# Kernel tuning notes

Measured on AMD Instinct MI355X. Metric: run time of the kernel, lower is better.

The kernel has to match this reference:

```python
import jax, jax.numpy as jnp
import numpy as np

B, T_ENC, T_OUT = 64, 1024, 1000
N_MELS, ENC_D, DEC_H, ATTN_D = 80, 256, 256, 256


def setup_inputs() -> dict:
    key = jax.random.key(0)
    ks = jax.random.split(key, 24)

    def p(k, shape, scale=0.05):
        return jax.random.normal(k, shape, dtype=jnp.float32) * scale

    lengths = jax.random.randint(ks[0], (B,), T_ENC // 2, T_ENC + 1)
    enc_mask = (jnp.arange(T_ENC)[None, :] < lengths[:, None]).astype(jnp.float32)
    return {
        "enc_outputs": jax.random.normal(ks[1], (B, T_ENC, ENC_D), dtype=jnp.float32),
        "target_mel": jax.random.normal(ks[2], (B, T_OUT, N_MELS), dtype=jnp.float32),
        # attention params
        "W_enc": p(ks[3], (ATTN_D, ENC_D)), "b_enc": jnp.zeros((ATTN_D,), jnp.float32),
        "W_dec": p(ks[4], (ATTN_D, DEC_H)), "b_dec": jnp.zeros((ATTN_D,), jnp.float32),
        "v_w": p(ks[5], (1, ATTN_D)), "v_b": jnp.zeros((1,), jnp.float32),
        # prenet
        "pre_W1": p(ks[6], (DEC_H, N_MELS)), "pre_b1": jnp.zeros((DEC_H,), jnp.float32),
        "pre_W2": p(ks[7], (DEC_H, DEC_H)), "pre_b2": jnp.zeros((DEC_H,), jnp.float32),
        # LSTMCell (PyTorch gate order i, f, g, o)
        "W_ih": p(ks[8], (4 * DEC_H, DEC_H + ENC_D)), "W_hh": p(ks[9], (4 * DEC_H, DEC_H)),
        "b_ih": jnp.zeros((4 * DEC_H,), jnp.float32), "b_hh": jnp.zeros((4 * DEC_H,), jnp.float32),
        # output heads
        "mel_W": p(ks[10], (N_MELS, DEC_H + ENC_D)), "mel_b": jnp.zeros((N_MELS,), jnp.float32),
        "stop_W": p(ks[11], (1, DEC_H + ENC_D)), "stop_b": jnp.zeros((1,), jnp.float32),
        "enc_mask": enc_mask,
    }


def reference(enc_outputs, target_mel, W_enc, b_enc, W_dec, b_dec, v_w, v_b,
              pre_W1, pre_b1, pre_W2, pre_b2, W_ih, W_hh, b_ih, b_hh,
              mel_W, mel_b, stop_W, stop_b, enc_mask):
    Bsz = enc_outputs.shape[0]
    H = W_hh.shape[1]
    NEG = jnp.float32(-1e9)
    # precompute encoder projection once, as the original does
    attn_enc = jnp.einsum('bte,ae->bta', enc_outputs, W_enc) + b_enc  # (B, T_enc, A)
    # teacher forcing: input at step t is target_mel[t-1], zeros at t=0
    prev_inputs = jnp.concatenate(
        [jnp.zeros_like(target_mel[:, :1]), target_mel[:, :-1]], axis=1)
    xs = jnp.swapaxes(prev_inputs, 0, 1)  # (T_out, B, n_mels)

    def step(carry, prev):
        h, c = carry
        attn_dec = h @ W_dec.T + b_dec                                  # (B, A)
        energy = jnp.tanh(attn_enc + attn_dec[:, None, :]) @ v_w[0] + v_b[0]  # (B, T_enc)
        energy = jnp.where(enc_mask == 0, NEG, energy)
        attn = jax.nn.softmax(energy, axis=-1)
        context = jnp.einsum('bt,btd->bd', attn, enc_outputs)           # (B, enc_d)
        pre = jax.nn.relu(prev @ pre_W1.T + pre_b1)                     # dropout = identity (eval)
        pre = jax.nn.relu(pre @ pre_W2.T + pre_b2)
        x = jnp.concatenate([pre, context], axis=1)
        gates = x @ W_ih.T + b_ih + h @ W_hh.T + b_hh                   # (B, 4H)
        i, f, g, o = jnp.split(gates, 4, axis=1)
        c_new = jax.nn.sigmoid(f) * c + jax.nn.sigmoid(i) * jnp.tanh(g)
        h_new = jax.nn.sigmoid(o) * jnp.tanh(c_new)
        comb = jnp.concatenate([h_new, context], axis=1)
        mel = comb @ mel_W.T + mel_b
        stop = (comb @ stop_W.T + stop_b)[:, 0]
        return (h_new, c_new), (mel, stop)

    h0 = jnp.zeros((Bsz, H), dtype=enc_outputs.dtype)
    _, (mels, stops) = jax.lax.scan(step, (h0, h0), xs)
    return jnp.swapaxes(mels, 0, 1), jnp.swapaxes(stops, 0, 1)
```

## Files before the change

kernel.cpp:

```cpp
#include <hip/hip_runtime.h>
#include <hip/hip_bf16.h>

#define NMEL 80

__device__ __forceinline__ float bf2f(unsigned short u) {
  unsigned v = ((unsigned)u) << 16; float f; __builtin_memcpy(&f, &v, 4); return f;
}
__device__ __forceinline__ unsigned short f2bf_u(float f) {
  __hip_bfloat16 h = __float2bfloat16(f); unsigned short u; __builtin_memcpy(&u, &h, 2); return u;
}
__device__ __forceinline__ float agload(const float* p) {
  return __hip_atomic_load(p, __ATOMIC_RELAXED, __HIP_MEMORY_SCOPE_AGENT);
}
__device__ __forceinline__ void agstore(float* p, float v) {
  __hip_atomic_store(p, v, __ATOMIC_RELAXED, __HIP_MEMORY_SCOPE_AGENT);
}
__device__ __forceinline__ void unpk(unsigned u, float& lo, float& hi) {
  unsigned l = u << 16, h = u & 0xffff0000u;
  __builtin_memcpy(&lo, &l, 4); __builtin_memcpy(&hi, &h, 4);
}
__device__ __forceinline__ void pin_u(unsigned& x) { asm volatile("" : "+v"(x)); }

constexpr size_t OFF_ATTNR = 0;
constexpr size_t SZ_ATTNR = (size_t)64 * 256 * 1024 * 2;
constexpr size_t OFF_ENCBF = OFF_ATTNR + SZ_ATTNR;
constexpr size_t SZ_ENCBF = (size_t)64 * 1024 * 256 * 2;
constexpr size_t OFF_PRE2 = OFF_ENCBF + SZ_ENCBF;
constexpr size_t SZ_PRE2 = (size_t)64000 * 256 * 2;
constexpr size_t OFF_WG4 = OFF_PRE2 + SZ_PRE2;
constexpr size_t SZ_W4 = (size_t)262144 * 4;
constexpr size_t OFF_WP4 = OFF_WG4 + SZ_W4;
constexpr size_t OFF_WHH4 = OFF_WP4 + SZ_W4;
constexpr size_t OFF_WDEC4 = OFF_WHH4 + SZ_W4;
constexpr size_t SZ_WDEC4 = (size_t)65536 * 4;
constexpr size_t OFF_MELT = OFF_WDEC4 + SZ_WDEC4;
constexpr size_t SZ_MELT = (size_t)4 * 128 * 80 * 4;
constexpr size_t OFF_STOPT = OFF_MELT + SZ_MELT;
constexpr size_t SZ_STOPT = (size_t)4 * 128 * 4;
constexpr size_t OFF_BIASG = OFF_STOPT + SZ_STOPT;
constexpr size_t SZ_BIASG = (size_t)4 * 256 * 4;
constexpr size_t OFF_EXCH = (OFF_BIASG + SZ_BIASG + 255) & ~(size_t)255;
constexpr size_t EXF_DEC = 0;
constexpr size_t EXN_DEC = (size_t)2 * 64 * 4 * 256;
constexpr size_t EXF_GH = EXF_DEC + EXN_DEC;
constexpr size_t EXN_GH = (size_t)2 * 64 * 4 * 1024;
constexpr size_t EXF_CTX = EXF_GH + EXN_GH;
constexpr size_t EXN_CTX = (size_t)64 * 4 * 256;
constexpr size_t EXF_S = EXF_CTX + EXN_CTX;
constexpr size_t EXN_S = 64 * 16;
constexpr size_t EXF_CTR = EXF_S + EXN_S;
constexpr size_t EXN_CTR = 64 * 16;
constexpr size_t EXCH_FLOATS = EXF_CTR + EXN_CTR;
constexpr size_t SZ_EXCH = EXCH_FLOATS * 4;
constexpr size_t WS_NEED = OFF_EXCH + SZ_EXCH;

__global__ __launch_bounds__(256) void conv_bf16(const float* __restrict__ in,
                                                 unsigned short* __restrict__ out, int n) {
  int i = (blockIdx.x * 256 + threadIdx.x) * 2;
  if (i < n) {
    float2 v = *(const float2*)(in + i);
    unsigned pair = (unsigned)f2bf_u(v.x) | ((unsigned)f2bf_u(v.y) << 16);
    *(unsigned*)(out + i) = pair;
  }
}

__global__ __launch_bounds__(256) void prep_weights(
    const float* __restrict__ W_ih, const float* __restrict__ W_hh,
    const float* __restrict__ W_dec, const float* __restrict__ mel_W,
    const float* __restrict__ stop_W, const float* __restrict__ b_ih,
    const float* __restrict__ b_hh,
    float* __restrict__ Wg4, float* __restrict__ Wp4,
    float* __restrict__ Whh4, float* __restrict__ Wdec4,
    float* __restrict__ MelT, float* __restrict__ StopT, float* __restrict__ biasG) {
  int idx = blockIdx.x * 256 + threadIdx.x;
  if (idx < 262144) {
    int q = idx & 3, r = (idx >> 2) & 255, kq = (idx >> 10) & 63, s = idx >> 16;
    int grow = ((r >> 6) << 8) + s * 64 + (r & 63);
    Wg4[idx] = W_ih[(size_t)grow * 512 + 256 + kq * 4 + q];
    Wp4[idx] = W_ih[(size_t)grow * 512 + kq * 4 + q];
  } else if (idx < 524288) {
    int i = idx - 262144;
    int q = i & 3, rr = (i >> 2) & 1023, hq = (i >> 12) & 15, s = i >> 16;
    Whh4[i] = W_hh[(size_t)rr * 256 + s * 64 + hq * 4 + q];
  } else if (idx < 589824) {
    int i = idx - 524288;
    int q = i & 3, a = (i >> 2) & 255, hq = (i >> 10) & 15, s = (i >> 14) & 3;
    Wdec4[i] = W_dec[(size_t)a * 256 + s * 64 + hq * 4 + q];
  } else if (idx < 589824 + 40960) {
    int k = idx - 589824;
    int m = k % 80, r = k / 80;
    int cc = r & 127, s = r >> 7;
    int col = (cc < 64) ? (s * 64 + cc) : (256 + s * 64 + (cc - 64));
    MelT[k] = mel_W[(size_t)m * 512 + col];
  } else if (idx < 589824 + 40960 + 512) {
    int k = idx - (589824 + 40960);
    int cc = k & 127, s = k >> 7;
    int col = (cc < 64) ? (s * 64 + cc) : (256 + s * 64 + (cc - 64));
    StopT[k] = stop_W[col];
  } else if (idx < 589824 + 40960 + 512 + 1024) {
    int k = idx - (589824 + 40960 + 512);
    int j = k & 255, s = k >> 8;
    int row = ((j >> 6) << 8) + s * 64 + (j & 63);
    biasG[k] = b_ih[row] + b_hh[row];
  }
}

__global__ __launch_bounds__(256) void attn_gemm(const float* __restrict__ enc,
                                                 const float* __restrict__ W_enc,
                                                 const float* __restrict__ b_enc,
                                                 unsigned* __restrict__ attnR) {
  __shared__ unsigned short Alds[64 * 260];
  const int tid = threadIdx.x;
  const int row0 = blockIdx.x * 64;
  const int wv = tid >> 6, lane = tid & 63, nb = wv * 64;
  for (int idx = tid; idx < 64 * 256; idx += 256) {
    int r = idx >> 8, k = idx & 255;
    Alds[r * 260 + k] = f2bf_u(enc[(size_t)(row0 + r) * 256 + k]);
  }
  __syncthreads();
  float acc[64];
#pragma unroll
  for (int n = 0; n < 64; ++n) acc[n] = b_enc[nb + n];
  for (int k8 = 0; k8 < 256; k8 += 8) {
    ushort4 ua = *(const ushort4*)&Alds[lane * 260 + k8];
    ushort4 ub = *(const ushort4*)&Alds[lane * 260 + k8 + 4];
    float a0 = bf2f(ua.x), a1 = bf2f(ua.y), a2 = bf2f(ua.z), a3 = bf2f(ua.w);
    float a4 = bf2f(ub.x), a5 = bf2f(ub.y), a6 = bf2f(ub.z), a7 = bf2f(ub.w);
#pragma unroll
    for (int n = 0; n < 64; ++n) {
      const float4* wp = (const float4*)(W_enc + (size_t)(nb + n) * 256 + k8);
      float4 w0 = wp[0], w1 = wp[1];
      acc[n] = fmaf(a0, w0.x, acc[n]); acc[n] = fmaf(a1, w0.y, acc[n]);
      acc[n] = fmaf(a2, w0.z, acc[n]); acc[n] = fmaf(a3, w0.w, acc[n]);
      acc[n] = fmaf(a4, w1.x, acc[n]); acc[n] = fmaf(a5, w1.y, acc[n]);
      acc[n] = fmaf(a6, w1.z, acc[n]); acc[n] = fmaf(a7, w1.w, acc[n]);
    }
  }
  const float CE = 2.8853900817779268f;
  const int b = row0 >> 10;
  const int te_g = (row0 & 1023) + lane;
  const int sl = te_g >> 8, te_loc = te_g & 255;
#pragma unroll
  for (int n = 0; n < 64; n += 2) {
    int a = nb + n;
    unsigned pair = (unsigned)f2bf_u(acc[n] * CE) | ((unsigned)f2bf_u(acc[n + 1] * CE) << 16);
    size_t u4 = ((((size_t)(b * 4 + sl) * 4 + (a >> 6)) * 8 + ((a >> 3) & 7)) * 256 + te_loc);
    attnR[u4 * 4 + ((a & 7) >> 1)] = pair;
  }
}

__global__ __launch_bounds__(256) void prenet_fused(const float* __restrict__ tmel,
                                                    const float* __restrict__ W1,
                                                    const float* __restrict__ b1,
                                                    const float* __restrict__ W2,
                                                    const float* __restrict__ b2,
                                                    unsigned short* __restrict__ pre2) {
  __shared__ unsigned short Alds[64 * 260];
  const int tid = threadIdx.x;
  const int row0 = blockIdx.x * 64;
  const int wv = tid >> 6, lane = tid & 63, nb = wv * 64;
  for (int idx = tid; idx < 64 * 80; idx += 256) {
    int r = idx / 80, k = idx - r * 80;
    int R = row0 + r;
    float v = (R % 1000 != 0) ? tmel[(size_t)(R - 1) * NMEL + k] : 0.f;
    Alds[r * 260 + k] = f2bf_u(v);
  }
  __syncthreads();
  float acc[64];
#pragma unroll
  for (int n = 0; n < 64; ++n) acc[n] = b1[nb + n];
  for (int k8 = 0; k8 < 80; k8 += 8) {
    ushort4 ua = *(const ushort4*)&Alds[lane * 260 + k8];
    ushort4 ub = *(const ushort4*)&Alds[lane * 260 + k8 + 4];
    float a0 = bf2f(ua.x), a1 = bf2f(ua.y), a2 = bf2f(ua.z), a3 = bf2f(ua.w);
    float a4 = bf2f(ub.x), a5 = bf2f(ub.y), a6 = bf2f(ub.z), a7 = bf2f(ub.w);
#pragma unroll
    for (int n = 0; n < 64; ++n) {
      const float4* wp = (const float4*)(W1 + (size_t)(nb + n) * 80 + k8);
      float4 w0 = wp[0], w1 = wp[1];
      acc[n] = fmaf(a0, w0.x, acc[n]); acc[n] = fmaf(a1, w0.y, acc[n]);
      acc[n] = fmaf(a2, w0.z, acc[n]); acc[n] = fmaf(a3, w0.w, acc[n]);
      acc[n] = fmaf(a4, w1.x, acc[n]); acc[n] = fmaf(a5, w1.y, acc[n]);
      acc[n] = fmaf(a6, w1.z, acc[n]); acc[n] = fmaf(a7, w1.w, acc[n]);
    }
  }
  __syncthreads();
#pragma unroll
  for (int n = 0; n < 64; ++n) Alds[lane * 260 + nb + n] = f2bf_u(fmaxf(acc[n], 0.f));
  __syncthreads();
#pragma unroll
  for (int n = 0; n < 64; ++n) acc[n] = b2[nb + n];
  for (int k8 = 0; k8 < 256; k8 += 8) {
    ushort4 ua = *(const ushort4*)&Alds[lane * 260 + k8];
    ushort4 ub = *(const ushort4*)&Alds[lane * 260 + k8 + 4];
    float a0 = bf2f(ua.x), a1 = bf2f(ua.y), a2 = bf2f(ua.z), a3 = bf2f(ua.w);
    float a4 = bf2f(ub.x), a5 = bf2f(ub.y), a6 = bf2f(ub.z), a7 = bf2f(ub.w);
#pragma unroll
    for (int n = 0; n < 64; ++n) {
      const float4* wp = (const float4*)(W2 + (size_t)(nb + n) * 256 + k8);
      float4 w0 = wp[0], w1 = wp[1];
      acc[n] = fmaf(a0, w0.x, acc[n]); acc[n] = fmaf(a1, w0.y, acc[n]);
      acc[n] = fmaf(a2, w0.z, acc[n]); acc[n] = fmaf(a3, w0.w, acc[n]);
      acc[n] = fmaf(a4, w1.x, acc[n]); acc[n] = fmaf(a5, w1.y, acc[n]);
      acc[n] = fmaf(a6, w1.z, acc[n]); acc[n] = fmaf(a7, w1.w, acc[n]);
    }
  }
  __syncthreads();
#pragma unroll
  for (int n = 0; n < 64; ++n) Alds[lane * 260 + nb + n] = f2bf_u(fmaxf(acc[n], 0.f));
  __syncthreads();
  for (int idx = tid; idx < 64 * 128; idx += 256) {
    int r = idx >> 7, k2 = (idx & 127) * 2;
    unsigned pair = (unsigned)Alds[r * 260 + k2] | ((unsigned)Alds[r * 260 + k2 + 1] << 16);
    *(unsigned*)(pre2 + (size_t)(row0 + r) * 256 + k2) = pair;
  }
}

__global__ __launch_bounds__(1024, 4) void decoder_loop(
    const unsigned* __restrict__ attnR, const unsigned short* __restrict__ encbf,
    const unsigned short* __restrict__ pre2,
    const float* __restrict__ Wg4, const float* __restrict__ Wp4,
    const float* __restrict__ Whh4, const float* __restrict__ Wdec4,
    const float* __restrict__ MelT, const float* __restrict__ StopT,
    const float* __restrict__ biasG,
    float* exch, unsigned* ctr,
    const float* __restrict__ b_dec, const float* __restrict__ v_w,
    const float* __restrict__ v_b, const float* __restrict__ enc_mask,
    const float* __restrict__ mel_b, const float* __restrict__ stop_b,
    float* out) {
  __shared__ __align__(16) float scratch[4096];
  __shared__ __align__(16) float melT_lds[10240];
  __shared__ float stopT_lds[128];
  __shared__ __align__(16) float dec_lds[256];
  __shared__ __align__(16) float v2_lds[256];
  __shared__ __align__(16) float p_lds[256];
  __shared__ __align__(16) float ctx_lds[256];
  __shared__ __align__(16) float pre_lds[256];
  __shared__ float gates_lds[256];
  __shared__ float c_lds[64], h_lds[64];
  __shared__ float red_lds[16];
  __shared__ float sv_lds;

  const int tid = threadIdx.x;
  const int b = blockIdx.x & 63, s = blockIdx.x >> 6;
  const int t8 = tid & 255;
  const int chunk = tid >> 8;
  const int lane = tid & 63, wid = tid >> 6;
  const int w = tid >> 6;
  const float CE = 2.8853900817779268f;
  const float L2E = 1.4426950408889634f;

  if (tid < 256) {
    v2_lds[tid] = -2.f * v_w[tid];
    if (tid < 64) c_lds[tid] = 0.f;
    float sp = v_w[tid];
    for (int m = 32; m; m >>= 1) sp += __shfl_xor(sp, m);
    if (lane == 0) red_lds[wid] = sp;
  }
  for (int i = tid; i < 10240; i += 1024) melT_lds[i] = MelT[(size_t)s * 10240 + i];
  if (tid >= 512 && tid < 640) stopT_lds[tid - 512] = StopT[s * 128 + (tid - 512)];
  __syncthreads();
  if (tid == 0) sv_lds = red_lds[0] + red_lds[1] + red_lds[2] + red_lds[3];
  __syncthreads();
  const float Sv = sv_lds;
  const float vb = v_b[0];
  const float maskv = (tid < 256) ? enc_mask[b * 1024 + s * 256 + tid] : 0.f;
  const float bdec_r = (tid < 256) ? b_dec[tid] : 0.f;
  const float biasg_r = (tid < 256) ? biasG[s * 256 + tid] : 0.f;

  uint4 attn_r4[8];
  {
    const uint4* apR = (const uint4*)attnR + (((size_t)(b * 4 + s) * 4 + chunk) * 8) * 256 + t8;
#pragma unroll
    for (int j = 0; j < 8; ++j) attn_r4[j] = apR[(size_t)j << 8];
  }
  uint2 enc_r2[16];
  {
    const uint2* epR = (const uint2*)encbf + ((size_t)(b * 1024 + s * 256 + w * 16)) * 64 + lane;
#pragma unroll
    for (int t = 0; t < 16; ++t) enc_r2[t] = epR[(size_t)t << 6];
  }
#pragma unroll
  for (int j = 0; j < 8; ++j) {
    pin_u(attn_r4[j].x); pin_u(attn_r4[j].y); pin_u(attn_r4[j].z); pin_u(attn_r4[j].w);
  }
#pragma unroll
  for (int t = 0; t < 16; ++t) { pin_u(enc_r2[t].x); pin_u(enc_r2[t].y); }

  const int grow = ((t8 >> 6) << 8) + s * 64 + (t8 & 63);
  const float4* wg4 = (const float4*)Wg4 + ((size_t)(s * 64 + chunk * 16)) * 256 + t8;
  const float4* wp4 = (const float4*)Wp4 + ((size_t)(s * 64 + chunk * 16)) * 256 + t8;
  const float4* wh4 = (const float4*)Whh4 + ((size_t)s) * 16384 + tid;
  const float4* wd4 = (const float4*)Wdec4 + ((size_t)(s * 16 + chunk * 4)) * 256 + t8;
  const unsigned short* pre2_b = pre2 + (size_t)b * 256000;

  float* decP = exch + EXF_DEC;
  float* ghP = exch + EXF_GH;
  float* ctxP = exch + EXF_CTX;
  float* sP = exch + EXF_S;
  unsigned* ctrb = ctr + b * 16;
  unsigned epoch = 0;

  for (int it = 0; it < 1000; ++it) {
    const int par = it & 1;
    const int pn = par ^ 1;
    float prefv = (tid < 256) ? bf2f(pre2_b[it * 256 + tid]) : 0.f;
    scratch[tid] = agload(decP + ((size_t)(par * 64 + b)) * 1024 + tid);
    __syncthreads();
    if (tid < 256)
      dec_lds[tid] = (bdec_r + scratch[tid] + scratch[256 + tid] + scratch[512 + tid] +
                      scratch[768 + tid]) * CE;
    __syncthreads();
    {
      float acc = 0.f;
#pragma unroll
      for (int j = 0; j < 8; ++j) {
        uint4 u = attn_r4[j];
        int ab = chunk * 64 + j * 8;
        float4 d0 = *(const float4*)&dec_lds[ab];
        float4 d1 = *(const float4*)&dec_lds[ab + 4];
        float4 v0 = *(const float4*)&v2_lds[ab];
        float4 v1 = *(const float4*)&v2_lds[ab + 4];
        float t0, t1, t2, t3, t4, t5, t6, t7;
        unpk(u.x, t0, t1); unpk(u.y, t2, t3); unpk(u.z, t4, t5); unpk(u.w, t6, t7);
        acc = fmaf(v0.x, __builtin_amdgcn_rcpf(1.f + __builtin_amdgcn_exp2f(t0 + d0.x)), acc);
        acc = fmaf(v0.y, __builtin_amdgcn_rcpf(1.f + __builtin_amdgcn_exp2f(t1 + d0.y)), acc);
        acc = fmaf(v0.z, __builtin_amdgcn_rcpf(1.f + __builtin_amdgcn_exp2f(t2 + d0.z)), acc);
        acc = fmaf(v0.w, __builtin_amdgcn_rcpf(1.f + __builtin_amdgcn_exp2f(t3 + d0.w)), acc);
        acc = fmaf(v1.x, __builtin_amdgcn_rcpf(1.f + __builtin_amdgcn_exp2f(t4 + d1.x)), acc);
        acc = fmaf(v1.y, __builtin_amdgcn_rcpf(1.f + __builtin_amdgcn_exp2f(t5 + d1.y)), acc);
        acc = fmaf(v1.z, __builtin_amdgcn_rcpf(1.f + __builtin_amdgcn_exp2f(t6 + d1.z)), acc);
        acc = fmaf(v1.w, __builtin_amdgcn_rcpf(1.f + __builtin_amdgcn_exp2f(t7 + d1.w)), acc);
      }
      scratch[tid] = acc;
    }
    __syncthreads();
    if (tid < 256) {
      float e = Sv + vb + scratch[t8] + scratch[256 + t8] + scratch[512 + t8] + scratch[768 + t8];
      float p = (maskv != 0.f) ? __builtin_amdgcn_exp2f(e * L2E) : 0.f;
      p_lds[t8] = p;
      float sp = p;
      for (int m = 32; m; m >>= 1) sp += __shfl_xor(sp, m);
      if (lane == 0) red_lds[wid] = sp;
    }
    __syncthreads();
    {
      float c0 = 0, c1 = 0, c2 = 0, c3 = 0;
#pragma unroll
      for (int t = 0; t < 16; ++t) {
        float pv = p_lds[w * 16 + t];
        float e0, e1, e2, e3;
        unpk(enc_r2[t].x, e0, e1);
        unpk(enc_r2[t].y, e2, e3);
        c0 = fmaf(pv, e0, c0); c1 = fmaf(pv, e1, c1);
        c2 = fmaf(pv, e2, c2); c3 = fmaf(pv, e3, c3);
      }
      float* cb = &scratch[w * 256 + lane * 4];
      cb[0] = c0; cb[1] = c1; cb[2] = c2; cb[3] = c3;
      if (tid < 256) pre_lds[tid] = prefv;
    }
    __syncthreads();
    if (tid < 256) {
      float cp = 0.f;
#pragma unroll
      for (int ww = 0; ww < 16; ++ww) cp += scratch[ww * 256 + t8];
      agstore(ctxP + ((size_t)b * 4 + s) * 256 + t8, cp);
    }
    if (tid == 0)
      agstore(sP + b * 16 + s, red_lds[0] + red_lds[1] + red_lds[2] + red_lds[3]);
    __threadfence();
    __syncthreads();
    if (tid == 0) {
      ++epoch;
      __hip_atomic_fetch_add(ctrb, 1u, __ATOMIC_RELEASE, __HIP_MEMORY_SCOPE_AGENT);
      while (__hip_atomic_load(ctrb, __ATOMIC_ACQUIRE, __HIP_MEMORY_SCOPE_AGENT) < 4u * epoch)
        __builtin_amdgcn_s_sleep(1);
    }
    __syncthreads();
    scratch[tid] = agload(ctxP + ((size_t)b * 4 + chunk) * 256 + t8);
    if (tid < 4) red_lds[8 + tid] = agload(sP + b * 16 + tid);
    __syncthreads();
    if (tid < 256) {
      float rS = 1.f / (red_lds[8] + red_lds[9] + red_lds[10] + red_lds[11]);
      ctx_lds[t8] = (scratch[t8] + scratch[256 + t8] + scratch[512 + t8] + scratch[768 + t8]) * rS;
    }
    __syncthreads();
    {
      float g = agload(ghP + ((size_t)(par * 64 + b)) * 4096 + chunk * 1024 + grow);
#pragma unroll 8
      for (int i = 0; i < 16; ++i) {
        float4 wv = wg4[(size_t)i << 8];
        float4 qv = wp4[(size_t)i << 8];
        int kb = chunk * 64 + i * 4;
        float4 x = *(const float4*)&ctx_lds[kb];
        float4 y = *(const float4*)&pre_lds[kb];
        g = fmaf(wv.x, x.x, g); g = fmaf(wv.y, x.y, g);
        g = fmaf(wv.z, x.z, g); g = fmaf(wv.w, x.w, g);
        g = fmaf(qv.x, y.x, g); g = fmaf(qv.y, y.y, g);
        g = fmaf(qv.z, y.z, g); g = fmaf(qv.w, y.w, g);
      }
      scratch[tid] = g;
    }
    __syncthreads();
    if (tid < 256)
      gates_lds[t8] = biasg_r + scratch[t8] + scratch[256 + t8] + scratch[512 + t8] +
                      scratch[768 + t8];
    __syncthreads();
    if (tid < 64) {
      float ii = gates_lds[tid], ff = gates_lds[64 + tid];
      float gg = gates_lds[128 + tid], oo = gates_lds[192 + tid];
      float c = c_lds[tid];
      float si = __builtin_amdgcn_rcpf(1.f + __builtin_amdgcn_exp2f(-ii * L2E));
      float sf = __builtin_amdgcn_rcpf(1.f + __builtin_amdgcn_exp2f(-ff * L2E));
      float so = __builtin_amdgcn_rcpf(1.f + __builtin_amdgcn_exp2f(-oo * L2E));
      float tg2 = 1.f - 2.f * __builtin_amdgcn_rcpf(1.f + __builtin_amdgcn_exp2f(gg * CE));
      float cn = sf * c + si * tg2;
      float tc = 1.f - 2.f * __builtin_amdgcn_rcpf(1.f + __builtin_amdgcn_exp2f(cn * CE));
      c_lds[tid] = cn;
      h_lds[tid] = so * tc;
    }
    __syncthreads();
    if (tid < 80) {
      float a = (s == 0) ? mel_b[tid] : 0.f;
#pragma unroll 8
      for (int cc = 0; cc < 128; ++cc) {
        float xv = (cc < 64) ? h_lds[cc] : ctx_lds[s * 64 + (cc - 64)];
        a = fmaf(melT_lds[cc * 80 + tid], xv, a);
      }
      atomicAdd(&out[(size_t)b * 80000 + it * 80 + tid], a);
    }
    if (tid >= 512 && tid < 640) {
      int cc = tid - 512;
      float xv = (cc < 64) ? h_lds[cc] : ctx_lds[s * 64 + (cc - 64)];
      float sv2 = stopT_lds[cc] * xv;
      for (int m = 32; m; m >>= 1) sv2 += __shfl_xor(sv2, m);
      if (lane == 0) red_lds[12 + ((tid - 512) >> 6)] = sv2;
    }
    {
      float gd = 0.f;
#pragma unroll
      for (int i = 0; i < 4; ++i) {
        float4 wv = wd4[(size_t)i << 8];
        int hb = chunk * 16 + i * 4;
        gd = fmaf(wv.x, h_lds[hb + 0], gd); gd = fmaf(wv.y, h_lds[hb + 1], gd);
        gd = fmaf(wv.z, h_lds[hb + 2], gd); gd = fmaf(wv.w, h_lds[hb + 3], gd);
      }
      float gh = 0.f;
#pragma unroll 8
      for (int hq = 0; hq < 16; ++hq) {
        float4 wv = wh4[(size_t)hq << 10];
        gh = fmaf(wv.x, h_lds[hq * 4 + 0], gh); gh = fmaf(wv.y, h_lds[hq * 4 + 1], gh);
        gh = fmaf(wv.z, h_lds[hq * 4 + 2], gh); gh = fmaf(wv.w, h_lds[hq * 4 + 3], gh);
      }
      agstore(ghP + ((size_t)(pn * 64 + b) * 4 + s) * 1024 + tid, gh);
      scratch[tid] = gd;
    }
    __syncthreads();
    if (tid < 256)
      agstore(decP + ((size_t)(pn * 64 + b) * 4 + s) * 256 + t8,
              scratch[t8] + scratch[256 + t8] + scratch[512 + t8] + scratch[768 + t8]);
    if (tid == 0) {
      float st = (s == 0) ? stop_b[0] : 0.f;
      atomicAdd(&out[(size_t)5120000 + b * 1000 + it], st + red_lds[12] + red_lds[13]);
    }
    __threadfence();
    __syncthreads();
    if (tid == 0) {
      ++epoch;
      __hip_atomic_fetch_add(ctrb, 1u, __ATOMIC_RELEASE, __HIP_MEMORY_SCOPE_AGENT);
      while (__hip_atomic_load(ctrb, __ATOMIC_ACQUIRE, __HIP_MEMORY_SCOPE_AGENT) < 4u * epoch)
        __builtin_amdgcn_s_sleep(1);
    }
    __syncthreads();
  }
}

extern "C" void kernel_launch(void* const* d_in, const int* in_sizes, int n_in,
                              void* d_out, int out_size, void* d_ws, size_t ws_size,
                              hipStream_t stream) {
  const float* enc = (const float*)d_in[0];
  const float* tmel = (const float*)d_in[1];
  const float* W_enc = (const float*)d_in[2];
  const float* b_enc = (const float*)d_in[3];
  const float* W_dec = (const float*)d_in[4];
  const float* b_dec = (const float*)d_in[5];
  const float* v_w = (const float*)d_in[6];
  const float* v_b = (const float*)d_in[7];
  const float* pW1 = (const float*)d_in[8];
  const float* pb1 = (const float*)d_in[9];
  const float* pW2 = (const float*)d_in[10];
  const float* pb2 = (const float*)d_in[11];
  const float* W_ih = (const float*)d_in[12];
  const float* W_hh = (const float*)d_in[13];
  const float* b_ih = (const float*)d_in[14];
  const float* b_hh = (const float*)d_in[15];
  const float* mel_W = (const float*)d_in[16];
  const float* mel_b = (const float*)d_in[17];
  const float* stop_W = (const float*)d_in[18];
  const float* stop_b = (const float*)d_in[19];
  const float* emask = (const float*)d_in[20];

  if (ws_size < WS_NEED) return;

  char* ws = (char*)d_ws;
  unsigned* attnR = (unsigned*)(ws + OFF_ATTNR);
  unsigned short* encbf = (unsigned short*)(ws + OFF_ENCBF);
  unsigned short* pre2 = (unsigned short*)(ws + OFF_PRE2);
  float* Wg4 = (float*)(ws + OFF_WG4);
  float* Wp4 = (float*)(ws + OFF_WP4);
  float* Whh4 = (float*)(ws + OFF_WHH4);
  float* Wdec4 = (float*)(ws + OFF_WDEC4);
  float* MelT = (float*)(ws + OFF_MELT);
  float* StopT = (float*)(ws + OFF_STOPT);
  float* biasG = (float*)(ws + OFF_BIASG);
  float* exch = (float*)(ws + OFF_EXCH);
  unsigned* ctr = (unsigned*)(exch + EXF_CTR);

  hipMemsetAsync(exch, 0, SZ_EXCH, stream);
  hipMemsetAsync(d_out, 0, (size_t)out_size * 4, stream);

  conv_bf16<<<32768, 256, 0, stream>>>(enc, encbf, 64 * 1024 * 256);
  prep_weights<<<2470, 256, 0, stream>>>(W_ih, W_hh, W_dec, mel_W, stop_W, b_ih, b_hh,
                                         Wg4, Wp4, Whh4, Wdec4, MelT, StopT, biasG);
  attn_gemm<<<1024, 256, 0, stream>>>(enc, W_enc, b_enc, attnR);
  prenet_fused<<<1000, 256, 0, stream>>>(tmel, pW1, pb1, pW2, pb2, pre2);
  decoder_loop<<<256, 1024, 0, stream>>>(attnR, encbf, pre2, Wg4, Wp4, Whh4, Wdec4,
                                         MelT, StopT, biasG, exch, ctr, b_dec, v_w, v_b,
                                         emask, mel_b, stop_b, (float*)d_out);
}
```

Measured before the change: 168.6 ms.

## Run each batch decoder in one workgroup, dropping cross-block counter barriers

Measured after the change: 178.2 ms. +5.7%, slower.

```diff
diff --git a/kernel.cpp b/kernel.cpp
--- a/kernel.cpp
+++ b/kernel.cpp
@@ -3,105 +3,75 @@
 
 #define NMEL 80
 
+typedef unsigned u32x4 __attribute__((ext_vector_type(4)));
+
 __device__ __forceinline__ float bf2f(unsigned short u) {
   unsigned v = ((unsigned)u) << 16; float f; __builtin_memcpy(&f, &v, 4); return f;
 }
 __device__ __forceinline__ unsigned short f2bf_u(float f) {
   __hip_bfloat16 h = __float2bfloat16(f); unsigned short u; __builtin_memcpy(&u, &h, 2); return u;
-}
-__device__ __forceinline__ float agload(const float* p) {
-  return __hip_atomic_load(p, __ATOMIC_RELAXED, __HIP_MEMORY_SCOPE_AGENT);
-}
-__device__ __forceinline__ void agstore(float* p, float v) {
-  __hip_atomic_store(p, v, __ATOMIC_RELAXED, __HIP_MEMORY_SCOPE_AGENT);
 }
 __device__ __forceinline__ void unpk(unsigned u, float& lo, float& hi) {
   unsigned l = u << 16, h = u & 0xffff0000u;
   __builtin_memcpy(&lo, &l, 4); __builtin_memcpy(&hi, &h, 4);
 }
-__device__ __forceinline__ void pin_u(unsigned& x) { asm volatile("" : "+v"(x)); }
 
 constexpr size_t OFF_ATTNR = 0;
-constexpr size_t SZ_ATTNR = (size_t)64 * 256 * 1024 * 2;
-constexpr size_t OFF_ENCBF = OFF_ATTNR + SZ_ATTNR;
-constexpr size_t SZ_ENCBF = (size_t)64 * 1024 * 256 * 2;
-constexpr size_t OFF_PRE2 = OFF_ENCBF + SZ_ENCBF;
+constexpr size_t SZ_ATTNR = (size_t)64 * 1024 * 256 * 2;
+constexpr size_t OFF_ENCP = OFF_ATTNR + SZ_ATTNR;
+constexpr size_t SZ_ENCP = (size_t)64 * 1024 * 256 * 2;
+constexpr size_t OFF_PRE2 = OFF_ENCP + SZ_ENCP;
 constexpr size_t SZ_PRE2 = (size_t)64000 * 256 * 2;
-constexpr size_t OFF_WG4 = OFF_PRE2 + SZ_PRE2;
-constexpr size_t SZ_W4 = (size_t)262144 * 4;
-constexpr size_t OFF_WP4 = OFF_WG4 + SZ_W4;
-constexpr size_t OFF_WHH4 = OFF_WP4 + SZ_W4;
-constexpr size_t OFF_WDEC4 = OFF_WHH4 + SZ_W4;
-constexpr size_t SZ_WDEC4 = (size_t)65536 * 4;
-constexpr size_t OFF_MELT = OFF_WDEC4 + SZ_WDEC4;
-constexpr size_t SZ_MELT = (size_t)4 * 128 * 80 * 4;
-constexpr size_t OFF_STOPT = OFF_MELT + SZ_MELT;
-constexpr size_t SZ_STOPT = (size_t)4 * 128 * 4;
-constexpr size_t OFF_BIASG = OFF_STOPT + SZ_STOPT;
-constexpr size_t SZ_BIASG = (size_t)4 * 256 * 4;
-constexpr size_t OFF_EXCH = (OFF_BIASG + SZ_BIASG + 255) & ~(size_t)255;
-constexpr size_t EXF_DEC = 0;
-constexpr size_t EXN_DEC = (size_t)2 * 64 * 4 * 256;
-constexpr size_t EXF_GH = EXF_DEC + EXN_DEC;
-constexpr size_t EXN_GH = (size_t)2 * 64 * 4 * 1024;
-constexpr size_t EXF_CTX = EXF_GH + EXN_GH;
-constexpr size_t EXN_CTX = (size_t)64 * 4 * 256;
-constexpr size_t EXF_S = EXF_CTX + EXN_CTX;
-constexpr size_t EXN_S = 64 * 16;
-constexpr size_t EXF_CTR = EXF_S + EXN_S;
-constexpr size_t EXN_CTR = 64 * 16;
-constexpr size_t EXCH_FLOATS = EXF_CTR + EXN_CTR;
-constexpr size_t SZ_EXCH = EXCH_FLOATS * 4;
-constexpr size_t WS_NEED = OFF_EXCH + SZ_EXCH;
-
-__global__ __launch_bounds__(256) void conv_bf16(const float* __restrict__ in,
-                                                 unsigned short* __restrict__ out, int n) {
-  int i = (blockIdx.x * 256 + threadIdx.x) * 2;
-  if (i < n) {
-    float2 v = *(const float2*)(in + i);
-    unsigned pair = (unsigned)f2bf_u(v.x) | ((unsigned)f2bf_u(v.y) << 16);
-    *(unsigned*)(out + i) = pair;
-  }
-}
-
-__global__ __launch_bounds__(256) void prep_weights(
-    const float* __restrict__ W_ih, const float* __restrict__ W_hh,
-    const float* __restrict__ W_dec, const float* __restrict__ mel_W,
-    const float* __restrict__ stop_W, const float* __restrict__ b_ih,
+constexpr size_t OFF_WDT = OFF_PRE2 + SZ_PRE2;
+constexpr size_t SZ_WDT = (size_t)65536 * 4;
+constexpr size_t OFF_WHT = OFF_WDT + SZ_WDT;
+constexpr size_t SZ_W1M = (size_t)262144 * 4;
+constexpr size_t OFF_WCT = OFF_WHT + SZ_W1M;
+constexpr size_t OFF_WPT = OFF_WCT + SZ_W1M;
+constexpr size_t OFF_BIASG = OFF_WPT + SZ_W1M;
+constexpr size_t SZ_BIASG = 1024 * 4;
+constexpr size_t WS_NEED = OFF_BIASG + SZ_BIASG;
+
+__global__ __launch_bounds__(256) void conv_encP(const float* __restrict__ enc,
+                                                 u32x4* __restrict__ encP) {
+  int idx = blockIdx.x * 256 + threadIdx.x;
+  int b = idx >> 15, r = idx & 32767;
+  int d8 = r >> 10, te = r & 1023;
+  const float4* src = (const float4*)(enc + ((size_t)(b * 1024 + te)) * 256 + d8 * 8);
+  float4 x0 = src[0], x1 = src[1];
+  u32x4 o;
+  o.x = (unsigned)f2bf_u(x0.x) | ((unsigned)f2bf_u(x0.y) << 16);
+  o.y = (unsigned)f2bf_u(x0.z) | ((unsigned)f2bf_u(x0.w) << 16);
+  o.z = (unsigned)f2bf_u(x1.x) | ((unsigned)f2bf_u(x1.y) << 16);
+  o.w = (unsigned)f2bf_u(x1.z) | ((unsigned)f2bf_u(x1.w) << 16);
+  encP[((size_t)(b * 32 + d8)) * 1024 + te] = o;
+}
+
+__global__ __launch_bounds__(256) void prep_w2(
+    const float* __restrict__ W_dec, const float* __restrict__ W_hh,
+    const float* __restrict__ W_ih, const float* __restrict__ b_ih,
     const float* __restrict__ b_hh,
-    float* __restrict__ Wg4, float* __restrict__ Wp4,
-    float* __restrict__ Whh4, float* __restrict__ Wdec4,
-    float* __restrict__ MelT, float* __restrict__ StopT, float* __restrict__ biasG) {
+    float* __restrict__ WdT, float* __restrict__ WhT,
+    float* __restrict__ WcT, float* __restrict__ WpT, float* __restrict__ biasG) {
   int idx = blockIdx.x * 256 + threadIdx.x;
-  if (idx < 262144) {
-    int q = idx & 3, r = (idx >> 2) & 255, kq = (idx >> 10) & 63, s = idx >> 16;
-    int grow = ((r >> 6) << 8) + s * 64 + (r & 63);
-    Wg4[idx] = W_ih[(size_t)grow * 512 + 256 + kq * 4 + q];
-    Wp4[idx] = W_ih[(size_t)grow * 512 + kq * 4 + q];
-  } else if (idx < 524288) {
-    int i = idx - 262144;
-    int q = i & 3, rr = (i >> 2) & 1023, hq = (i >> 12) & 15, s = i >> 16;
-    Whh4[i] = W_hh[(size_t)rr * 256 + s * 64 + hq * 4 + q];
+  if (idx < 65536) {
+    int q = idx & 3, a = (idx >> 2) & 255, kq = idx >> 10;
+    WdT[idx] = W_dec[(size_t)a * 256 + kq * 4 + q];
+  } else if (idx < 327680) {
+    int i = idx - 65536;
+    int q = i & 3, g = (i >> 2) & 1023, kq = i >> 12;
+    WhT[i] = W_hh[(size_t)g * 256 + kq * 4 + q];
   } else if (idx < 589824) {
-    int i = idx - 524288;
-    int q = i & 3, a = (i >> 2) & 255, hq = (i >> 10) & 15, s = (i >> 14) & 3;
-    Wdec4[i] = W_dec[(size_t)a * 256 + s * 64 + hq * 4 + q];
-  } else if (idx < 589824 + 40960) {
-    int k = idx - 589824;
-    int m = k % 80, r = k / 80;
-    int cc = r & 127, s = r >> 7;
-    int col = (cc < 64) ? (s * 64 + cc) : (256 + s * 64 + (cc - 64));
-    MelT[k] = mel_W[(size_t)m * 512 + col];
-  } else if (idx < 589824 + 40960 + 512) {
-    int k = idx - (589824 + 40960);
-    int cc = k & 127, s = k >> 7;
-    int col = (cc < 64) ? (s * 64 + cc) : (256 + s * 64 + (cc - 64));
-    StopT[k] = stop_W[col];
-  } else if (idx < 589824 + 40960 + 512 + 1024) {
-    int k = idx - (589824 + 40960 + 512);
-    int j = k & 255, s = k >> 8;
-    int row = ((j >> 6) << 8) + s * 64 + (j & 63);
-    biasG[k] = b_ih[row] + b_hh[row];
+    int i = idx - 327680;
+    int q = i & 3, g = (i >> 2) & 1023, kq = i >> 12;
+    WcT[i] = W_ih[(size_t)g * 512 + 256 + kq * 4 + q];
+  } else if (idx < 851968) {
+    int i = idx - 589824;
+    int q = i & 3, g = (i >> 2) & 1023, kq = i >> 12;
+    WpT[i] = W_ih[(size_t)g * 512 + kq * 4 + q];
+  } else if (idx < 852992) {
+    int g = idx - 851968;
+    biasG[g] = b_ih[g] + b_hh[g];
   }
 }
 
@@ -216,107 +186,122 @@
   }
 }
 
-__global__ __launch_bounds__(1024, 4) void decoder_loop(
-    const unsigned* __restrict__ attnR, const unsigned short* __restrict__ encbf,
+__global__ __launch_bounds__(1024, 4) void decoder_one(
+    const u32x4* __restrict__ attnR, const u32x4* __restrict__ encP,
     const unsigned short* __restrict__ pre2,
-    const float* __restrict__ Wg4, const float* __restrict__ Wp4,
-    const float* __restrict__ Whh4, const float* __restrict__ Wdec4,
-    const float* __restrict__ MelT, const float* __restrict__ StopT,
+    const float4* __restrict__ WdT, const float4* __restrict__ WhT,
+    const float4* __restrict__ WcT, const float4* __restrict__ WpT,
     const float* __restrict__ biasG,
-    float* exch, unsigned* ctr,
     const float* __restrict__ b_dec, const float* __restrict__ v_w,
     const float* __restrict__ v_b, const float* __restrict__ enc_mask,
-    const float* __restrict__ mel_b, const float* __restrict__ stop_b,
-    float* out) {
-  __shared__ __align__(16) float scratch[4096];
-  __shared__ __align__(16) float melT_lds[10240];
-  __shared__ float stopT_lds[128];
+    const float* __restrict__ mel_W, const float* __restrict__ mel_b,
+    const float* __restrict__ stop_W, const float* __restrict__ stop_b,
+    float* __restrict__ out) {
+  __shared__ __align__(16) float scratchB[8448];
+  __shared__ __align__(16) float p_lds[1024];
+  __shared__ __align__(16) float gates_lds[1024];
+  __shared__ __align__(16) float h_lds[256];
+  __shared__ __align__(16) float ctx_lds[256];
+  __shared__ __align__(16) float pre_lds[256];
   __shared__ __align__(16) float dec_lds[256];
   __shared__ __align__(16) float v2_lds[256];
-  __shared__ __align__(16) float p_lds[256];
-  __shared__ __align__(16) float ctx_lds[256];
-  __shared__ __align__(16) float pre_lds[256];
-  __shared__ float gates_lds[256];
-  __shared__ float c_lds[64], h_lds[64];
   __shared__ float red_lds[16];
-  __shared__ float sv_lds;
 
   const int tid = threadIdx.x;
-  const int b = blockIdx.x & 63, s = blockIdx.x >> 6;
-  const int t8 = tid & 255;
-  const int chunk = tid >> 8;
+  const int b = blockIdx.x;
+  const int t8 = tid & 255, chunk = tid >> 8;
   const int lane = tid & 63, wid = tid >> 6;
-  const int w = tid >> 6;
+  const int d8 = tid >> 5, tec = tid & 31;
   const float CE = 2.8853900817779268f;
   const float L2E = 1.4426950408889634f;
 
   if (tid < 256) {
-    v2_lds[tid] = -2.f * v_w[tid];
-    if (tid < 64) c_lds[tid] = 0.f;
-    float sp = v_w[tid];
-    for (int m = 32; m; m >>= 1) sp += __shfl_xor(sp, m);
-    if (lane == 0) red_lds[wid] = sp;
-  }
-  for (int i = tid; i < 10240; i += 1024) melT_lds[i] = MelT[(size_t)s * 10240 + i];
-  if (tid >= 512 && tid < 640) stopT_lds[tid - 512] = StopT[s * 128 + (tid - 512)];
-  __syncthreads();
-  if (tid == 0) sv_lds = red_lds[0] + red_lds[1] + red_lds[2] + red_lds[3];
-  __syncthreads();
-  const float Sv = sv_lds;
-  const float vb = v_b[0];
-  const float maskv = (tid < 256) ? enc_mask[b * 1024 + s * 256 + tid] : 0.f;
+    h_lds[tid] = 0.f;
+    float v = v_w[tid];
+    v2_lds[tid] = -2.f * v;
+    for (int m = 32; m; m >>= 1) v += __shfl_xor(v, m);
+    if (lane == 0) red_lds[wid] = v;
+  }
+  float c_reg = 0.f;
+  const float maskv = enc_mask[b * 1024 + tid];
   const float bdec_r = (tid < 256) ? b_dec[tid] : 0.f;
-  const float biasg_r = (tid < 256) ? biasG[s * 256 + tid] : 0.f;
-
-  uint4 attn_r4[8];
-  {
-    const uint4* apR = (const uint4*)attnR + (((size_t)(b * 4 + s) * 4 + chunk) * 8) * 256 + t8;
-#pragma unroll
-    for (int j = 0; j < 8; ++j) attn_r4[j] = apR[(size_t)j << 8];
-  }
-  uint2 enc_r2[16];
-  {
-    const uint2* epR = (const uint2*)encbf + ((size_t)(b * 1024 + s * 256 + w * 16)) * 64 + lane;
-#pragma unroll
-    for (int t = 0; t < 16; ++t) enc_r2[t] = epR[(size_t)t << 6];
-  }
-#pragma unroll
-  for (int j = 0; j < 8; ++j) {
-    pin_u(attn_r4[j].x); pin_u(attn_r4[j].y); pin_u(attn_r4[j].z); pin_u(attn_r4[j].w);
-  }
-#pragma unroll
-  for (int t = 0; t < 16; ++t) { pin_u(enc_r2[t].x); pin_u(enc_r2[t].y); }
-
-  const int grow = ((t8 >> 6) << 8) + s * 64 + (t8 & 63);
-  const float4* wg4 = (const float4*)Wg4 + ((size_t)(s * 64 + chunk * 16)) * 256 + t8;
-  const float4* wp4 = (const float4*)Wp4 + ((size_t)(s * 64 + chunk * 16)) * 256 + t8;
-  const float4* wh4 = (const float4*)Whh4 + ((size_t)s) * 16384 + tid;
-  const float4* wd4 = (const float4*)Wdec4 + ((size_t)(s * 16 + chunk * 4)) * 256 + t8;
+  const float biasg_r = biasG[tid];
+  const float melb_r = (tid < 640 && (tid & 7) == 0) ? mel_b[tid >> 3] : 0.f;
+  float stopw[8];
+  if (wid == 11) {
+#pragma unroll
+    for (int i = 0; i < 8; ++i) stopw[i] = stop_W[lane * 8 + i];
+  }
+  __syncthreads();
+  const float Sv_vb = red_lds[0] + red_lds[1] + red_lds[2] + red_lds[3] + v_b[0];
+  const float stopb0 = stop_b[0];
+
+  const u32x4* aB = attnR + (size_t)b * 32768 + chunk * 2048 + t8;
+  const u32x4* eB = encP + ((size_t)(b * 32 + d8)) * 1024 + tec;
+  const float4* wdB = WdT + chunk * 16 * 256 + t8;
+  const float4* whB = WhT + tid;
+  const float4* wcB = WcT + tid;
+  const float4* wpB = WpT + tid;
   const unsigned short* pre2_b = pre2 + (size_t)b * 256000;
-
-  float* decP = exch + EXF_DEC;
-  float* ghP = exch + EXF_GH;
-  float* ctxP = exch + EXF_CTX;
-  float* sP = exch + EXF_S;
-  unsigned* ctrb = ctr + b * 16;
-  unsigned epoch = 0;
+  float* outm = out + (size_t)b * 80000;
+  float* outs = out + (size_t)5120000 + b * 1000;
+
+  auto heads = [&](int ith) {
+    if (tid < 640) {
+      const int m = tid >> 3, q = tid & 7;
+      float acc = melb_r;
+      const float4* wm = (const float4*)(mel_W + (size_t)m * 512 + q * 64);
+      const float4* xp = (q < 4) ? (const float4*)&h_lds[q * 64]
+                                 : (const float4*)&ctx_lds[(q - 4) * 64];
+#pragma unroll
+      for (int i = 0; i < 16; ++i) {
+        float4 w = wm[i]; float4 x = xp[i];
+        acc = fmaf(w.x, x.x, acc); acc = fmaf(w.y, x.y, acc);
+        acc = fmaf(w.z, x.z, acc); acc = fmaf(w.w, x.w, acc);
+      }
+      acc += __shfl_xor(acc, 1); acc += __shfl_xor(acc, 2); acc += __shfl_xor(acc, 4);
+      if (q == 0) outm[ith * 80 + m] = acc;
+    } else if (wid == 11) {
+      float acc = 0.f;
+#pragma unroll
+      for (int i = 0; i < 8; ++i) {
+        int cc = lane * 8 + i;
+        float x = (cc < 256) ? h_lds[cc] : ctx_lds[cc - 256];
+        acc = fmaf(stopw[i], x, acc);
+      }
+      for (int m = 32; m; m >>= 1) acc += __shfl_xor(acc, m);
+      if (lane == 0) outs[ith] = acc + stopb0;
+    }
+  };
+
+  float gph = 0.f;
 
   for (int it = 0; it < 1000; ++it) {
-    const int par = it & 1;
-    const int pn = par ^ 1;
-    float prefv = (tid < 256) ? bf2f(pre2_b[it * 256 + tid]) : 0.f;
-    scratch[tid] = agload(decP + ((size_t)(par * 64 + b)) * 1024 + tid);
-    __syncthreads();
-    if (tid < 256)
-      dec_lds[tid] = (bdec_r + scratch[tid] + scratch[256 + tid] + scratch[512 + tid] +
-                      scratch[768 + tid]) * CE;
-    __syncthreads();
     {
       float acc = 0.f;
 #pragma unroll
+      for (int i = 0; i < 16; ++i) {
+        float4 w = wdB[(size_t)i << 8];
+        float4 h4 = *(const float4*)&h_lds[chunk * 64 + i * 4];
+        acc = fmaf(w.x, h4.x, acc); acc = fmaf(w.y, h4.y, acc);
+        acc = fmaf(w.z, h4.z, acc); acc = fmaf(w.w, h4.w, acc);
+      }
+      scratchB[(chunk << 8) + t8] = acc;
+      if (tid < 256) pre_lds[tid] = bf2f(pre2_b[it * 256 + tid]);
+      if (it > 0) heads(it - 1);
+    }
+    __syncthreads();
+    if (tid < 256)
+      dec_lds[tid] = (bdec_r + scratchB[tid] + scratchB[256 + tid] +
+                      scratchB[512 + tid] + scratchB[768 + tid]) * CE;
+    __syncthreads();
+#pragma unroll 1
+    for (int sl = 0; sl < 4; ++sl) {
+      float acc = 0.f;
+#pragma unroll
       for (int j = 0; j < 8; ++j) {
-        uint4 u = attn_r4[j];
-        int ab = chunk * 64 + j * 8;
+        u32x4 u = __builtin_nontemporal_load(&aB[sl * 8192 + j * 256]);
+        int ab = (chunk << 6) + (j << 3);
         float4 d0 = *(const float4*)&dec_lds[ab];
         float4 d1 = *(const float4*)&dec_lds[ab + 4];
         float4 v0 = *(const float4*)&v2_lds[ab];
@@ -332,147 +317,99 @@
         acc = fmaf(v1.z, __builtin_amdgcn_rcpf(1.f + __builtin_amdgcn_exp2f(t6 + d1.z)), acc);
         acc = fmaf(v1.w, __builtin_amdgcn_rcpf(1.f + __builtin_amdgcn_exp2f(t7 + d1.w)), acc);
       }
-      scratch[tid] = acc;
+      scratchB[sl * 1024 + (chunk << 8) + t8] = acc;
+    }
+    __syncthreads();
+    {
+      int base = (tid >> 8) * 1024 + (tid & 255);
+      float e = Sv_vb + scratchB[base] + scratchB[base + 256] +
+                scratchB[base + 512] + scratchB[base + 768];
+      float p = (maskv != 0.f) ? __builtin_amdgcn_exp2f(e * L2E) : 0.f;
+      p_lds[tid] = p;
+      for (int m = 32; m; m >>= 1) p += __shfl_xor(p, m);
+      if (lane == 0) red_lds[wid] = p;
+    }
+    __syncthreads();
+    {
+      gph = biasg_r;
+      float cc0 = 0, cc1 = 0, cc2 = 0, cc3 = 0, cc4 = 0, cc5 = 0, cc6 = 0, cc7 = 0;
+      u32x4 eb[8];
+      auto issueQ = [&](int q0) {
+#pragma unroll
+        for (int t = 0; t < 8; ++t)
+          eb[t] = __builtin_nontemporal_load(&eB[((q0 << 3) + t) << 5]);
+      };
+      auto consumeQ = [&](int q0) {
+#pragma unroll
+        for (int t = 0; t < 8; ++t) {
+          float pv = p_lds[((((q0 << 3) + t) << 5)) + tec];
+          float e0, e1, e2, e3, e4, e5, e6, e7;
+          unpk(eb[t].x, e0, e1); unpk(eb[t].y, e2, e3);
+          unpk(eb[t].z, e4, e5); unpk(eb[t].w, e6, e7);
+          cc0 = fmaf(pv, e0, cc0); cc1 = fmaf(pv, e1, cc1);
+          cc2 = fmaf(pv, e2, cc2); cc3 = fmaf(pv, e3, cc3);
+          cc4 = fmaf(pv, e4, cc4); cc5 = fmaf(pv, e5, cc5);
+          cc6 = fmaf(pv, e6, cc6); cc7 = fmaf(pv, e7, cc7);
+        }
+      };
+      auto gdot = [&](const float4* __restrict__ wB, const float* __restrict__ xl, int i0) {
+#pragma unroll 8
+        for (int i = i0; i < i0 + 32; ++i) {
+          float4 w = wB[(size_t)i << 10];
+          float4 x = *(const float4*)&xl[i << 2];
+          gph = fmaf(w.x, x.x, gph); gph = fmaf(w.y, x.y, gph);
+          gph = fmaf(w.z, x.z, gph); gph = fmaf(w.w, x.w, gph);
+        }
+      };
+      issueQ(0); gdot(wpB, pre_lds, 0);  consumeQ(0);
+      issueQ(1); gdot(wpB, pre_lds, 32); consumeQ(1);
+      issueQ(2); gdot(whB, h_lds, 0);    consumeQ(2);
+      issueQ(3); gdot(whB, h_lds, 32);   consumeQ(3);
+      float* cb = &scratchB[(d8 << 3) * 33 + tec];
+      cb[0] = cc0; cb[33] = cc1; cb[66] = cc2; cb[99] = cc3;
+      cb[132] = cc4; cb[165] = cc5; cb[198] = cc6; cb[231] = cc7;
     }
     __syncthreads();
     if (tid < 256) {
-      float e = Sv + vb + scratch[t8] + scratch[256 + t8] + scratch[512 + t8] + scratch[768 + t8];
-      float p = (maskv != 0.f) ? __builtin_amdgcn_exp2f(e * L2E) : 0.f;
-      p_lds[t8] = p;
-      float sp = p;
-      for (int m = 32; m; m >>= 1) sp += __shfl_xor(sp, m);
-      if (lane == 0) red_lds[wid] = sp;
+      float S = red_lds[0] + red_lds[1] + red_lds[2] + red_lds[3] +
+                red_lds[4] + red_lds[5] + red_lds[6] + red_lds[7] +
+                red_lds[8] + red_lds[9] + red_lds[10] + red_lds[11] +
+                red_lds[12] + red_lds[13] + red_lds[14] + red_lds[15];
+      float rS = 1.f / S;
+      float s = 0.f;
+      const float* row = &scratchB[tid * 33];
+#pragma unroll
+      for (int t = 0; t < 32; ++t) s += row[t];
+      ctx_lds[tid] = s * rS;
     }
     __syncthreads();
     {
-      float c0 = 0, c1 = 0, c2 = 0, c3 = 0;
-#pragma unroll
-      for (int t = 0; t < 16; ++t) {
-        float pv = p_lds[w * 16 + t];
-        float e0, e1, e2, e3;
-        unpk(enc_r2[t].x, e0, e1);
-        unpk(enc_r2[t].y, e2, e3);
-        c0 = fmaf(pv, e0, c0); c1 = fmaf(pv, e1, c1);
-        c2 = fmaf(pv, e2, c2); c3 = fmaf(pv, e3, c3);
+      float g = gph;
+#pragma unroll 8
+      for (int i = 0; i < 64; ++i) {
+        float4 w = wcB[(size_t)i << 10];
+        float4 x = *(const float4*)&ctx_lds[i << 2];
+        g = fmaf(w.x, x.x, g); g = fmaf(w.y, x.y, g);
+        g = fmaf(w.z, x.z, g); g = fmaf(w.w, x.w, g);
       }
-      float* cb = &scratch[w * 256 + lane * 4];
-      cb[0] = c0; cb[1] = c1; cb[2] = c2; cb[3] = c3;
-      if (tid < 256) pre_lds[tid] = prefv;
+      gates_lds[tid] = g;
     }
     __syncthreads();
     if (tid < 256) {
-      float cp = 0.f;
-#pragma unroll
-      for (int ww = 0; ww < 16; ++ww) cp += scratch[ww * 256 + t8];
-      agstore(ctxP + ((size_t)b * 4 + s) * 256 + t8, cp);
-    }
-    if (tid == 0)
-      agstore(sP + b * 16 + s, red_lds[0] + red_lds[1] + red_lds[2] + red_lds[3]);
-    __threadfence();
-    __syncthreads();
-    if (tid == 0) {
-      ++epoch;
-      __hip_atomic_fetch_add(ctrb, 1u, __ATOMIC_RELEASE, __HIP_MEMORY_SCOPE_AGENT);
-      while (__hip_atomic_load(ctrb, __ATOMIC_ACQUIRE, __HIP_MEMORY_SCOPE_AGENT) < 4u * epoch)
-        __builtin_amdgcn_s_sleep(1);
-    }
-    __syncthreads();
-    scratch[tid] = agload(ctxP + ((size_t)b * 4 + chunk) * 256 + t8);
-    if (tid < 4) red_lds[8 + tid] = agload(sP + b * 16 + tid);
-    __syncthreads();
-    if (tid < 256) {
-      float rS = 1.f / (red_lds[8] + red_lds[9] + red_lds[10] + red_lds[11]);
-      ctx_lds[t8] = (scratch[t8] + scratch[256 + t8] + scratch[512 + t8] + scratch[768 + t8]) * rS;
-    }
-    __syncthreads();
-    {
-      float g = agload(ghP + ((size_t)(par * 64 + b)) * 4096 + chunk * 1024 + grow);
-#pragma unroll 8
-      for (int i = 0; i < 16; ++i) {
-        float4 wv = wg4[(size_t)i << 8];
-        float4 qv = wp4[(size_t)i << 8];
-        int kb = chunk * 64 + i * 4;
-        float4 x = *(const float4*)&ctx_lds[kb];
-        float4 y = *(const float4*)&pre_lds[kb];
-        g = fmaf(wv.x, x.x, g); g = fmaf(wv.y, x.y, g);
-        g = fmaf(wv.z, x.z, g); g = fmaf(wv.w, x.w, g);
-        g = fmaf(qv.x, y.x, g); g = fmaf(qv.y, y.y, g);
-        g = fmaf(qv.z, y.z, g); g = fmaf(qv.w, y.w, g);
-      }
-      scratch[tid] = g;
-    }
-    __syncthreads();
-    if (tid < 256)
-      gates_lds[t8] = biasg_r + scratch[t8] + scratch[256 + t8] + scratch[512 + t8] +
-                      scratch[768 + t8];
-    __syncthreads();
-    if (tid < 64) {
-      float ii = gates_lds[tid], ff = gates_lds[64 + tid];
-      float gg = gates_lds[128 + tid], oo = gates_lds[192 + tid];
-      float c = c_lds[tid];
+      float ii = gates_lds[tid], ff = gates_lds[256 + tid];
+      float gg = gates_lds[512 + tid], oo = gates_lds[768 + tid];
       float si = __builtin_amdgcn_rcpf(1.f + __builtin_amdgcn_exp2f(-ii * L2E));
       float sf = __builtin_amdgcn_rcpf(1.f + __builtin_amdgcn_exp2f(-ff * L2E));
       float so = __builtin_amdgcn_rcpf(1.f + __builtin_amdgcn_exp2f(-oo * L2E));
       float tg2 = 1.f - 2.f * __builtin_amdgcn_rcpf(1.f + __builtin_amdgcn_exp2f(gg * CE));
-      float cn = sf * c + si * tg2;
+      float cn = sf * c_reg + si * tg2;
       float tc = 1.f - 2.f * __builtin_amdgcn_rcpf(1.f + __builtin_amdgcn_exp2f(cn * CE));
-      c_lds[tid] = cn;
+      c_reg = cn;
       h_lds[tid] = so * tc;
     }
     __syncthreads();
-    if (tid < 80) {
-      float a = (s == 0) ? mel_b[tid] : 0.f;
-#pragma unroll 8
-      for (int cc = 0; cc < 128; ++cc) {
-        float xv = (cc < 64) ? h_lds[cc] : ctx_lds[s * 64 + (cc - 64)];
-        a = fmaf(melT_lds[cc * 80 + tid], xv, a);
-      }
-      atomicAdd(&out[(size_t)b * 80000 + it * 80 + tid], a);
-    }
-    if (tid >= 512 && tid < 640) {
-      int cc = tid - 512;
-      float xv = (cc < 64) ? h_lds[cc] : ctx_lds[s * 64 + (cc - 64)];
-      float sv2 = stopT_lds[cc] * xv;
-      for (int m = 32; m; m >>= 1) sv2 += __shfl_xor(sv2, m);
-      if (lane == 0) red_lds[12 + ((tid - 512) >> 6)] = sv2;
-    }
-    {
-      float gd = 0.f;
-#pragma unroll
-      for (int i = 0; i < 4; ++i) {
-        float4 wv = wd4[(size_t)i << 8];
-        int hb = chunk * 16 + i * 4;
-        gd = fmaf(wv.x, h_lds[hb + 0], gd); gd = fmaf(wv.y, h_lds[hb + 1], gd);
-        gd = fmaf(wv.z, h_lds[hb + 2], gd); gd = fmaf(wv.w, h_lds[hb + 3], gd);
-      }
-      float gh = 0.f;
-#pragma unroll 8
-      for (int hq = 0; hq < 16; ++hq) {
-        float4 wv = wh4[(size_t)hq << 10];
-        gh = fmaf(wv.x, h_lds[hq * 4 + 0], gh); gh = fmaf(wv.y, h_lds[hq * 4 + 1], gh);
-        gh = fmaf(wv.z, h_lds[hq * 4 + 2], gh); gh = fmaf(wv.w, h_lds[hq * 4 + 3], gh);
-      }
-      agstore(ghP + ((size_t)(pn * 64 + b) * 4 + s) * 1024 + tid, gh);
-      scratch[tid] = gd;
-    }
-    __syncthreads();
-    if (tid < 256)
-      agstore(decP + ((size_t)(pn * 64 + b) * 4 + s) * 256 + t8,
-              scratch[t8] + scratch[256 + t8] + scratch[512 + t8] + scratch[768 + t8]);
-    if (tid == 0) {
-      float st = (s == 0) ? stop_b[0] : 0.f;
-      atomicAdd(&out[(size_t)5120000 + b * 1000 + it], st + red_lds[12] + red_lds[13]);
-    }
-    __threadfence();
-    __syncthreads();
-    if (tid == 0) {
-      ++epoch;
-      __hip_atomic_fetch_add(ctrb, 1u, __ATOMIC_RELEASE, __HIP_MEMORY_SCOPE_AGENT);
-      while (__hip_atomic_load(ctrb, __ATOMIC_ACQUIRE, __HIP_MEMORY_SCOPE_AGENT) < 4u * epoch)
-        __builtin_amdgcn_s_sleep(1);
-    }
-    __syncthreads();
-  }
+  }
+  heads(999);
 }
 
 extern "C" void kernel_launch(void* const* d_in, const int* in_sizes, int n_in,
@@ -504,27 +441,20 @@
 
   char* ws = (char*)d_ws;
   unsigned* attnR = (unsigned*)(ws + OFF_ATTNR);
-  unsigned short* encbf = (unsigned short*)(ws + OFF_ENCBF);
+  u32x4* encP = (u32x4*)(ws + OFF_ENCP);
   unsigned short* pre2 = (unsigned short*)(ws + OFF_PRE2);
-  float* Wg4 = (float*)(ws + OFF_WG4);
-  float* Wp4 = (float*)(ws + OFF_WP4);
-  float* Whh4 = (float*)(ws + OFF_WHH4);
-  float* Wdec4 = (float*)(ws + OFF_WDEC4);
-  float* MelT = (float*)(ws + OFF_MELT);
-  float* StopT = (float*)(ws + OFF_STOPT);
+  float* WdT = (float*)(ws + OFF_WDT);
+  float* WhT = (float*)(ws + OFF_WHT);
+  float* WcT = (float*)(ws + OFF_WCT);
+  float* WpT = (float*)(ws + OFF_WPT);
   float* biasG = (float*)(ws + OFF_BIASG);
-  float* exch = (float*)(ws + OFF_EXCH);
-  unsigned* ctr = (unsigned*)(exch + EXF_CTR);
-
-  hipMemsetAsync(exch, 0, SZ_EXCH, stream);
-  hipMemsetAsync(d_out, 0, (size_t)out_size * 4, stream);
-
-  conv_bf16<<<32768, 256, 0, stream>>>(enc, encbf, 64 * 1024 * 256);
-  prep_weights<<<2470, 256, 0, stream>>>(W_ih, W_hh, W_dec, mel_W, stop_W, b_ih, b_hh,
-                                         Wg4, Wp4, Whh4, Wdec4, MelT, StopT, biasG);
+
+  conv_encP<<<8192, 256, 0, stream>>>(enc, encP);
+  prep_w2<<<3332, 256, 0, stream>>>(W_dec, W_hh, W_ih, b_ih, b_hh, WdT, WhT, WcT, WpT, biasG);
   attn_gemm<<<1024, 256, 0, stream>>>(enc, W_enc, b_enc, attnR);
   prenet_fused<<<1000, 256, 0, stream>>>(tmel, pW1, pb1, pW2, pb2, pre2);
-  decoder_loop<<<256, 1024, 0, stream>>>(attnR, encbf, pre2, Wg4, Wp4, Whh4, Wdec4,
-                                         MelT, StopT, biasG, exch, ctr, b_dec, v_w, v_b,
-                                         emask, mel_b, stop_b, (float*)d_out);
-}
+  decoder_one<<<64, 1024, 0, stream>>>(
+      (const u32x4*)attnR, (const u32x4*)encP, pre2,
+      (const float4*)WdT, (const float4*)WhT, (const float4*)WcT, (const float4*)WpT,
+      biasG, b_dec, v_w, v_b, emask, mel_W, mel_b, stop_W, stop_b, (float*)d_out);
+}
```
